# Kernel optimization log

Measured on AMD Instinct MI355X. Metric: run time of the kernel, lower is better.

## Reference

```python
import jax, jax.numpy as jnp
import numpy as np

B, S, E, D = 8, 2048, 1024, 64

def setup_inputs() -> dict:
    key = jax.random.key(0)
    k1, k2, k3, k4 = jax.random.split(key, 4)
    x = jax.random.normal(k1, (B, S, E), dtype=jnp.float32)
    attention_mask = jnp.ones((B, S, S), dtype=jnp.int32)
    scale = 1.0 / np.sqrt(E)
    Wq = jax.random.normal(k2, (E, D), dtype=jnp.float32) * scale
    Wk = jax.random.normal(k3, (E, D), dtype=jnp.float32) * scale
    Wv = jax.random.normal(k4, (E, D), dtype=jnp.float32) * scale
    return {"x": x, "attention_mask": attention_mask, "Wq": Wq, "Wk": Wk, "Wv": Wv}

def reference(x, attention_mask, Wq, Wk, Wv):
    # Q,K,V projections: [B,S,E] @ [E,D] -> [B,S,D]
    Q = jnp.einsum('bse,ed->bsd', x, Wq)
    K = jnp.einsum('bse,ed->bsd', x, Wk)
    V = jnp.einsum('bse,ed->bsd', x, Wv)
    d_head = Q.shape[-1]
    # scores: [B,S,S], scaled by sqrt(dim_head)
    scores = jnp.einsum('bqd,bkd->bqk', Q, K) / jnp.sqrt(jnp.asarray(d_head, Q.dtype))
    scores = jnp.where(attention_mask == 0, jnp.asarray(-jnp.inf, scores.dtype), scores)
    attn = jax.nn.softmax(scores, axis=-1)
    # dropout p=0.0 (eval mode) -> identity
    out = jnp.einsum('bqk,bkd->bqd', attn, V)
    return out
```

## Files before the change

kernel.cpp:

```cpp
#include <hip/hip_runtime.h>
#include <hip/hip_bf16.h>
#include <math.h>


typedef __attribute__((ext_vector_type(8))) short short8;
typedef __attribute__((ext_vector_type(4))) float v4f;

__device__ __forceinline__ unsigned short f2bf(float f) {
  unsigned int u = __float_as_uint(f);
  unsigned int r = (u + 0x7fffu + ((u >> 16) & 1u)) >> 16;
  return (unsigned short)r;
}

__global__ __launch_bounds__(256) void prep_wf(const float* __restrict__ Wq,
                                               const float* __restrict__ Wk,
                                               const float* __restrict__ Wv,
                                               unsigned short* __restrict__ Wf) {
  int o = blockIdx.x * 256 + threadIdx.x;
  int j = o & 7;
  int lane = (o >> 3) & 63;
  int c = o >> 9;
  int kk = c & 1;
  int nt = (c % 24) >> 1;
  int kt = c / 24;
  int q = lane & 15, quad = lane >> 4;
  int n = nt * 16 + q;
  int k = kt * 64 + kk * 32 + quad * 8 + j;
  const float* W = (n < 64) ? Wq : (n < 128 ? Wk : Wv);
  Wf[o] = f2bf(W[(size_t)k * 64 + (n & 63)]);
}

__global__ __launch_bounds__(512) void proj_kernel(const float* __restrict__ x,
                                                   const unsigned short* __restrict__ Wf,
                                                   unsigned short* __restrict__ Qg,
                                                   unsigned short* __restrict__ Kf,
                                                   unsigned short* __restrict__ Vf) {
  const int tid = threadIdx.x;
  const int w = tid >> 6;
  const int lane = tid & 63;
  const int q = lane & 15, quad = lane >> 4;
  const int rg = w >> 2, ng = w & 3;
  const int m0 = blockIdx.x * 32 + rg * 16;

  const float* xrow = x + (size_t)(m0 + q) * 1024 + quad * 8;
  const unsigned short* Wl = Wf + lane * 8;

  v4f acc[3];
#pragma unroll
  for (int i = 0; i < 3; i++) acc[i] = (v4f)(0.0f);

  float4 acur[4], anext[4];
  auto loadA = [&](int kt, float4 a[4]) {
    const float* p = xrow + kt * 64;
    a[0] = *reinterpret_cast<const float4*>(p);
    a[1] = *reinterpret_cast<const float4*>(p + 4);
    a[2] = *reinterpret_cast<const float4*>(p + 32);
    a[3] = *reinterpret_cast<const float4*>(p + 36);
  };

  loadA(0, acur);

  for (int kt = 0; kt < 16; kt++) {
    if (kt < 15) loadA(kt + 1, anext);
    short8 af0, af1;
    {
      float* f = reinterpret_cast<float*>(acur);
#pragma unroll
      for (int j = 0; j < 4; j++) { af0[j] = (short)f2bf(f[j]); af0[4 + j] = (short)f2bf(f[4 + j]); }
#pragma unroll
      for (int j = 0; j < 4; j++) { af1[j] = (short)f2bf(f[8 + j]); af1[4 + j] = (short)f2bf(f[12 + j]); }
    }
    __builtin_amdgcn_s_setprio(1);
#pragma unroll
    for (int i = 0; i < 3; i++) {
      const size_t toff = ((size_t)kt * 24 + (ng * 3 + i) * 2) * 512;
      short8 b0 = *reinterpret_cast<const short8*>(Wl + toff);
      short8 b1 = *reinterpret_cast<const short8*>(Wl + toff + 512);
      acc[i] = __builtin_amdgcn_mfma_f32_16x16x32_bf16(af0, b0, acc[i], 0, 0, 0);
      acc[i] = __builtin_amdgcn_mfma_f32_16x16x32_bf16(af1, b1, acc[i], 0, 0, 0);
    }
    __builtin_amdgcn_s_setprio(0);
#pragma unroll
    for (int i = 0; i < 4; i++) acur[i] = anext[i];
  }

#pragma unroll
  for (int i = 0; i < 3; i++) {
    const int n = (ng * 3 + i) * 16 + q;
#pragma unroll
    for (int r = 0; r < 4; r++) {
      const int m = m0 + quad * 4 + r;
      const unsigned short hv = f2bf(acc[i][r]);
      if (n < 64) {
        Qg[(size_t)m * 64 + n] = hv;
      } else if (n < 128) {
        const int d = n - 64, s = m;
        const int b = s >> 11, srem = s & 2047, g = srem >> 4, qi = srem & 15;
        const int kk2 = d >> 5, quad2 = (d >> 3) & 3, j2 = d & 7;
        Kf[((((size_t)b * 128 + g) * 2 + kk2) * 64 + quad2 * 16 + qi) * 8 + j2] = hv;
      } else {
        const int d = n - 128, s = m;
        const int b = s >> 11, srem = s & 2047, kt2 = srem >> 6, s6 = srem & 63;
        const int kk2 = s6 >> 5, quad2 = (s6 >> 3) & 3, j2 = s6 & 7;
        const int dt = d >> 4, qi = d & 15;
        Vf[(((((size_t)b * 32 + kt2) * 4 + dt) * 2 + kk2) * 64 + quad2 * 16 + qi) * 8 + j2] = hv;
      }
    }
  }
}

__global__ __launch_bounds__(256, 3) void attn_kernel(const unsigned short* __restrict__ Qg,
                                                      const unsigned short* __restrict__ Kf,
                                                      const unsigned short* __restrict__ Vf,
                                                      const int* __restrict__ maskg,
                                                      float* __restrict__ outg) {
  __shared__ __align__(16) unsigned short Pl[4][16][72];

  const int tid = threadIdx.x;
  const int bid = blockIdx.x;
  const int b = bid & 7, qt = bid >> 3;
  const int q0 = qt * 16;
  const int w = tid >> 6, lane = tid & 63;
  const int q = lane & 15, quad = lane >> 4;

  const size_t qbase = ((size_t)b * 2048 + q0 + q) * 64 + quad * 8;
  const short8 qf0 = *reinterpret_cast<const short8*>(&Qg[qbase]);
  const short8 qf1 = *reinterpret_cast<const short8*>(&Qg[qbase + 32]);

  short8 onesf;
#pragma unroll
  for (int j = 0; j < 8; j++) onesf[j] = (short)0x3F80;

  const unsigned short* Kb = Kf + (size_t)b * 131072 + lane * 8;
  const unsigned short* Vb = Vf + (size_t)b * 131072 + lane * 8;
  const int* mb = maskg + ((size_t)b * 2048 + q0 + quad) * 2048 + q * 4;

  v4f o_acc[4], l_acc;
#pragma unroll
  for (int dt = 0; dt < 4; dt++) o_acc[dt] = (v4f)(0.0f);
  l_acc = (v4f)(0.0f);

  const float SC = 0.125f * 1.4426950408889634f;
  const int kt0 = w * 8;

  unsigned zb = 0;
  {
    int4 m4[4];
#pragma unroll
    for (int j = 0; j < 4; j++)
      m4[j] = *reinterpret_cast<const int4*>(mb + (size_t)j * 8192 + kt0 * 64);
#pragma unroll
    for (int j = 0; j < 4; j++)
      zb |= ((unsigned)(m4[j].x == 0) << (j * 4)) | ((unsigned)(m4[j].y == 0) << (j * 4 + 1)) |
            ((unsigned)(m4[j].z == 0) << (j * 4 + 2)) | ((unsigned)(m4[j].w == 0) << (j * 4 + 3));
  }

#pragma unroll
  for (int it = 0; it < 8; it++) {
    const int kt = kt0 + it;

    int4 m4[4];
    if (it < 7) {
#pragma unroll
      for (int j = 0; j < 4; j++)
        m4[j] = *reinterpret_cast<const int4*>(mb + (size_t)j * 8192 + (kt + 1) * 64);
    }

    v4f s_acc[4];
    __builtin_amdgcn_s_setprio(1);
#pragma unroll
    for (int nt = 0; nt < 4; nt++) {
      short8 k0 = *reinterpret_cast<const short8*>(Kb + ((size_t)kt * 8 + nt * 2 + 0) * 512);
      short8 k1 = *reinterpret_cast<const short8*>(Kb + ((size_t)kt * 8 + nt * 2 + 1) * 512);
      s_acc[nt] = __builtin_amdgcn_mfma_f32_16x16x32_bf16(qf0, k0, (v4f)(0.0f), 0, 0, 0);
      s_acc[nt] = __builtin_amdgcn_mfma_f32_16x16x32_bf16(qf1, k1, s_acc[nt], 0, 0, 0);
    }
    __builtin_amdgcn_s_setprio(0);

#pragma unroll
    for (int nt = 0; nt < 4; nt++)
#pragma unroll
      for (int r = 0; r < 4; r++)
        Pl[w][quad * 4 + r][nt * 16 + q] = f2bf(exp2f(s_acc[nt][r] * SC));

    if (__any(zb != 0u)) {
#pragma unroll
      for (int j = 0; j < 4; j++)
#pragma unroll
        for (int c = 0; c < 4; c++)
          if ((zb >> (j * 4 + c)) & 1u) Pl[w][j * 4 + quad][q * 4 + c] = 0;
    }

    const short8 pf0 = *reinterpret_cast<const short8*>(&Pl[w][q][quad * 8]);
    const short8 pf1 = *reinterpret_cast<const short8*>(&Pl[w][q][32 + quad * 8]);

    __builtin_amdgcn_s_setprio(1);
#pragma unroll
    for (int dt = 0; dt < 4; dt++) {
      short8 v0 = *reinterpret_cast<const short8*>(Vb + ((size_t)kt * 8 + dt * 2 + 0) * 512);
      short8 v1 = *reinterpret_cast<const short8*>(Vb + ((size_t)kt * 8 + dt * 2 + 1) * 512);
      o_acc[dt] = __builtin_amdgcn_mfma_f32_16x16x32_bf16(pf0, v0, o_acc[dt], 0, 0, 0);
      o_acc[dt] = __builtin_amdgcn_mfma_f32_16x16x32_bf16(pf1, v1, o_acc[dt], 0, 0, 0);
    }
    l_acc = __builtin_amdgcn_mfma_f32_16x16x32_bf16(pf0, onesf, l_acc, 0, 0, 0);
    l_acc = __builtin_amdgcn_mfma_f32_16x16x32_bf16(pf1, onesf, l_acc, 0, 0, 0);
    __builtin_amdgcn_s_setprio(0);

    if (it < 7) {
      zb = 0;
#pragma unroll
      for (int j = 0; j < 4; j++)
        zb |= ((unsigned)(m4[j].x == 0) << (j * 4)) | ((unsigned)(m4[j].y == 0) << (j * 4 + 1)) |
              ((unsigned)(m4[j].z == 0) << (j * 4 + 2)) | ((unsigned)(m4[j].w == 0) << (j * 4 + 3));
    }
  }

  __syncthreads();
  float* Osf = reinterpret_cast<float*>(&Pl[0][0][0]);
  float* Lsf = Osf + 2 * 16 * 68;

  if (w >= 2) {
    const int wi = w - 2;
#pragma unroll
    for (int r = 0; r < 4; r++) {
      const int row = quad * 4 + r;
#pragma unroll
      for (int dt = 0; dt < 4; dt++) Osf[(wi * 16 + row) * 68 + dt * 16 + q] = o_acc[dt][r];
      if (q == 0) Lsf[wi * 16 + row] = l_acc[r];
    }
  }
  __syncthreads();
  if (w < 2) {
#pragma unroll
    for (int r = 0; r < 4; r++) {
      const int row = quad * 4 + r;
#pragma unroll
      for (int dt = 0; dt < 4; dt++) o_acc[dt][r] += Osf[(w * 16 + row) * 68 + dt * 16 + q];
      l_acc[r] += Lsf[w * 16 + row];
    }
  }
  __syncthreads();
  if (w == 1) {
#pragma unroll
    for (int r = 0; r < 4; r++) {
      const int row = quad * 4 + r;
#pragma unroll
      for (int dt = 0; dt < 4; dt++) Osf[row * 68 + dt * 16 + q] = o_acc[dt][r];
      if (q == 0) Lsf[row] = l_acc[r];
    }
  }
  __syncthreads();
  if (w == 0) {
#pragma unroll
    for (int r = 0; r < 4; r++) {
      const int row = quad * 4 + r;
      const float inv = 1.0f / (l_acc[r] + Lsf[row]);
      const size_t orow = ((size_t)b * 2048 + q0 + row) * 64;
#pragma unroll
      for (int dt = 0; dt < 4; dt++)
        outg[orow + dt * 16 + q] = (o_acc[dt][r] + Osf[row * 68 + dt * 16 + q]) * inv;
    }
  }
}

extern "C" void kernel_launch(void* const* d_in, const int* in_sizes, int n_in,
                              void* d_out, int out_size, void* d_ws, size_t ws_size,
                              hipStream_t stream) {
  const float* x = (const float*)d_in[0];
  const int* mask = (const int*)d_in[1];
  const float* Wq = (const float*)d_in[2];
  const float* Wk = (const float*)d_in[3];
  const float* Wv = (const float*)d_in[4];
  float* out = (float*)d_out;

  char* ws = (char*)d_ws;
  unsigned short* Qg = (unsigned short*)(ws);
  unsigned short* Kf = (unsigned short*)(ws + (size_t)(2 << 20));
  unsigned short* Vf = (unsigned short*)(ws + (size_t)(4 << 20));
  unsigned short* Wf = (unsigned short*)(ws + (size_t)(6 << 20));

  prep_wf<<<768, 256, 0, stream>>>(Wq, Wk, Wv, Wf);
  proj_kernel<<<512, 512, 0, stream>>>(x, Wf, Qg, Kf, Vf);
  attn_kernel<<<1024, 256, 0, stream>>>(Qg, Kf, Vf, mask, out);
}
```

Measured before the change: 301.2 us.

## Prefetch weight, K and V fragments into registers; vectorize weight prep

The projection kernel now double-buffers the bf16 weight fragments in registers, loading the next k-tile alongside the next x tile. The attention kernel prefetches the next K tile after the score MFMAs and issues the V loads before the softmax/exp stage, so global-load latency overlaps with compute. The weight-prep kernel reads float4 rows (four outputs per thread, quarter the blocks) instead of gathering scalars. Together these raise register pressure, which may lower occupancy.

```diff
diff --git a/kernel.cpp b/kernel.cpp
--- a/kernel.cpp
+++ b/kernel.cpp
@@ -16,18 +16,24 @@
                                                const float* __restrict__ Wk,
                                                const float* __restrict__ Wv,
                                                unsigned short* __restrict__ Wf) {
-  int o = blockIdx.x * 256 + threadIdx.x;
-  int j = o & 7;
-  int lane = (o >> 3) & 63;
-  int c = o >> 9;
-  int kk = c & 1;
-  int nt = (c % 24) >> 1;
-  int kt = c / 24;
-  int q = lane & 15, quad = lane >> 4;
-  int n = nt * 16 + q;
-  int k = kt * 64 + kk * 32 + quad * 8 + j;
-  const float* W = (n < 64) ? Wq : (n < 128 ? Wk : Wv);
-  Wf[o] = f2bf(W[(size_t)k * 64 + (n & 63)]);
+  int t = blockIdx.x * 256 + threadIdx.x;
+  int e0 = t * 4;
+  int m = e0 >> 16;
+  int rem = e0 & 65535;
+  int k = rem >> 6, n0 = rem & 63;
+  const float* W = (m == 0) ? Wq : (m == 1 ? Wk : Wv);
+  float4 f4 = *reinterpret_cast<const float4*>(W + rem);
+  int kt = k >> 6, rr = k & 63;
+  int kk = rr >> 5, quad = (rr >> 3) & 3, j = k & 7;
+  int cbase = kt * 24 + kk;
+  float f[4] = {f4.x, f4.y, f4.z, f4.w};
+#pragma unroll
+  for (int c = 0; c < 4; c++) {
+    int N = m * 64 + n0 + c;
+    int nt = N >> 4, q = N & 15;
+    int o = (((cbase + nt * 2) << 6) | (quad * 16 + q)) * 8 + j;
+    Wf[o] = f2bf(f[c]);
+  }
 }
 
 __global__ __launch_bounds__(512) void proj_kernel(const float* __restrict__ x,
@@ -58,10 +64,24 @@
     a[3] = *reinterpret_cast<const float4*>(p + 36);
   };
 
+  short8 bcur[6], bnext[6];
+  auto loadB = [&](int kt, short8 bb[6]) {
+#pragma unroll
+    for (int i = 0; i < 3; i++) {
+      const size_t toff = ((size_t)kt * 24 + (ng * 3 + i) * 2) * 512;
+      bb[2 * i + 0] = *reinterpret_cast<const short8*>(Wl + toff);
+      bb[2 * i + 1] = *reinterpret_cast<const short8*>(Wl + toff + 512);
+    }
+  };
+
   loadA(0, acur);
+  loadB(0, bcur);
 
   for (int kt = 0; kt < 16; kt++) {
-    if (kt < 15) loadA(kt + 1, anext);
+    if (kt < 15) {
+      loadA(kt + 1, anext);
+      loadB(kt + 1, bnext);
+    }
     short8 af0, af1;
     {
       float* f = reinterpret_cast<float*>(acur);
@@ -73,15 +93,14 @@
     __builtin_amdgcn_s_setprio(1);
 #pragma unroll
     for (int i = 0; i < 3; i++) {
-      const size_t toff = ((size_t)kt * 24 + (ng * 3 + i) * 2) * 512;
-      short8 b0 = *reinterpret_cast<const short8*>(Wl + toff);
-      short8 b1 = *reinterpret_cast<const short8*>(Wl + toff + 512);
-      acc[i] = __builtin_amdgcn_mfma_f32_16x16x32_bf16(af0, b0, acc[i], 0, 0, 0);
-      acc[i] = __builtin_amdgcn_mfma_f32_16x16x32_bf16(af1, b1, acc[i], 0, 0, 0);
+      acc[i] = __builtin_amdgcn_mfma_f32_16x16x32_bf16(af0, bcur[2 * i + 0], acc[i], 0, 0, 0);
+      acc[i] = __builtin_amdgcn_mfma_f32_16x16x32_bf16(af1, bcur[2 * i + 1], acc[i], 0, 0, 0);
     }
     __builtin_amdgcn_s_setprio(0);
 #pragma unroll
     for (int i = 0; i < 4; i++) acur[i] = anext[i];
+#pragma unroll
+    for (int i = 0; i < 6; i++) bcur[i] = bnext[i];
   }
 
 #pragma unroll
@@ -143,6 +162,12 @@
   const float SC = 0.125f * 1.4426950408889634f;
   const int kt0 = w * 8;
 
+  auto loadK = [&](int kt, short8 kk[8]) {
+#pragma unroll
+    for (int f = 0; f < 8; f++)
+      kk[f] = *reinterpret_cast<const short8*>(Kb + ((size_t)kt * 8 + f) * 512);
+  };
+
   unsigned zb = 0;
   {
     int4 m4[4];
@@ -155,6 +180,9 @@
             ((unsigned)(m4[j].z == 0) << (j * 4 + 2)) | ((unsigned)(m4[j].w == 0) << (j * 4 + 3));
   }
 
+  short8 kcur[8], knext[8];
+  loadK(kt0, kcur);
+
 #pragma unroll
   for (int it = 0; it < 8; it++) {
     const int kt = kt0 + it;
@@ -170,12 +198,17 @@
     __builtin_amdgcn_s_setprio(1);
 #pragma unroll
     for (int nt = 0; nt < 4; nt++) {
-      short8 k0 = *reinterpret_cast<const short8*>(Kb + ((size_t)kt * 8 + nt * 2 + 0) * 512);
-      short8 k1 = *reinterpret_cast<const short8*>(Kb + ((size_t)kt * 8 + nt * 2 + 1) * 512);
-      s_acc[nt] = __builtin_amdgcn_mfma_f32_16x16x32_bf16(qf0, k0, (v4f)(0.0f), 0, 0, 0);
-      s_acc[nt] = __builtin_amdgcn_mfma_f32_16x16x32_bf16(qf1, k1, s_acc[nt], 0, 0, 0);
+      s_acc[nt] = __builtin_amdgcn_mfma_f32_16x16x32_bf16(qf0, kcur[nt * 2 + 0], (v4f)(0.0f), 0, 0, 0);
+      s_acc[nt] = __builtin_amdgcn_mfma_f32_16x16x32_bf16(qf1, kcur[nt * 2 + 1], s_acc[nt], 0, 0, 0);
     }
     __builtin_amdgcn_s_setprio(0);
+
+    if (it < 7) loadK(kt + 1, knext);
+
+    short8 vf[8];
+#pragma unroll
+    for (int f = 0; f < 8; f++)
+      vf[f] = *reinterpret_cast<const short8*>(Vb + ((size_t)kt * 8 + f) * 512);
 
 #pragma unroll
     for (int nt = 0; nt < 4; nt++)
@@ -197,16 +230,16 @@
     __builtin_amdgcn_s_setprio(1);
 #pragma unroll
     for (int dt = 0; dt < 4; dt++) {
-      short8 v0 = *reinterpret_cast<const short8*>(Vb + ((size_t)kt * 8 + dt * 2 + 0) * 512);
-      short8 v1 = *reinterpret_cast<const short8*>(Vb + ((size_t)kt * 8 + dt * 2 + 1) * 512);
-      o_acc[dt] = __builtin_amdgcn_mfma_f32_16x16x32_bf16(pf0, v0, o_acc[dt], 0, 0, 0);
-      o_acc[dt] = __builtin_amdgcn_mfma_f32_16x16x32_bf16(pf1, v1, o_acc[dt], 0, 0, 0);
+      o_acc[dt] = __builtin_amdgcn_mfma_f32_16x16x32_bf16(pf0, vf[dt * 2 + 0], o_acc[dt], 0, 0, 0);
+      o_acc[dt] = __builtin_amdgcn_mfma_f32_16x16x32_bf16(pf1, vf[dt * 2 + 1], o_acc[dt], 0, 0, 0);
     }
     l_acc = __builtin_amdgcn_mfma_f32_16x16x32_bf16(pf0, onesf, l_acc, 0, 0, 0);
     l_acc = __builtin_amdgcn_mfma_f32_16x16x32_bf16(pf1, onesf, l_acc, 0, 0, 0);
     __builtin_amdgcn_s_setprio(0);
 
     if (it < 7) {
+#pragma unroll
+      for (int f = 0; f < 8; f++) kcur[f] = knext[f];
       zb = 0;
 #pragma unroll
       for (int j = 0; j < 4; j++)
@@ -279,7 +312,7 @@
   unsigned short* Vf = (unsigned short*)(ws + (size_t)(4 << 20));
   unsigned short* Wf = (unsigned short*)(ws + (size_t)(6 << 20));
 
-  prep_wf<<<768, 256, 0, stream>>>(Wq, Wk, Wv, Wf);
+  prep_wf<<<192, 256, 0, stream>>>(Wq, Wk, Wv, Wf);
   proj_kernel<<<512, 512, 0, stream>>>(x, Wf, Qg, Kf, Vf);
   attn_kernel<<<1024, 256, 0, stream>>>(Qg, Kf, Vf, mask, out);
 }
```

Result: faster. 295.0 us (-2.1%).
